# Kernel tuning notes

Measured on AMD Instinct MI355X. Metric: run time of the kernel, lower is better.

Reference implementation:

```python
import jax, jax.numpy as jnp
import numpy as np

N = 50000
ALPHA = 0.1
LAMDA = 0.5


def setup_inputs() -> dict:
    key = jax.random.key(0)
    ks = jax.random.split(key, 8)
    E, IN, H, C, L = 800000, 512, 128, 40, 8
    features = jax.random.normal(ks[0], (N, IN), dtype=jnp.float32)
    edge_index = jax.random.randint(ks[1], (2, E), 0, N, dtype=jnp.int32)
    norm_A = jax.random.uniform(ks[2], (E,), dtype=jnp.float32) * 0.1
    w_fc0 = jax.random.normal(ks[3], (IN, H), dtype=jnp.float32) / np.sqrt(IN)
    b_fc0 = jnp.zeros((H,), dtype=jnp.float32)
    conv_w = jax.random.normal(ks[4], (L, H, H), dtype=jnp.float32) / np.sqrt(H)
    w_fc1 = jax.random.normal(ks[5], (H, C), dtype=jnp.float32) / np.sqrt(H)
    b_fc1 = jnp.zeros((C,), dtype=jnp.float32)
    return {"features": features, "edge_index": edge_index, "norm_A": norm_A,
            "w_fc0": w_fc0, "b_fc0": b_fc0, "conv_w": conv_w,
            "w_fc1": w_fc1, "b_fc1": b_fc1}


def _spmm(edge_index, w, x):
    # y[dst] += w_e * x[src]  over all edges; x: [N, H]
    src, dst = edge_index[0], edge_index[1]
    msgs = x[src] * w[:, None]                      # [E, H]
    return jax.ops.segment_sum(msgs, dst, num_segments=N)


def reference(features, edge_index, norm_A, w_fc0, b_fc0, conv_w, w_fc1, b_fc1):
    # dropout p=0.0 -> identity
    x = jax.nn.relu(features @ w_fc0 + b_fc0)       # [N, H]
    h0 = x
    L = conv_w.shape[0]
    for i in range(L):
        l = i + 1
        beta = jnp.log(LAMDA / l + 1.0).astype(x.dtype)
        hi = _spmm(edge_index, norm_A, x)           # Â x
        support = (1.0 - ALPHA) * hi + ALPHA * h0   # initial residual
        # identity mapping: beta * (support W) + (1-beta) * support
        x = jax.nn.relu(beta * (support @ conv_w[i]) + (1.0 - beta) * support)
    return x @ w_fc1 + b_fc1                        # [N, C]
```

## Files before the change

### kernel.cpp

```cpp
#include <hip/hip_runtime.h>
#include <hip/hip_bf16.h>
#include <math.h>

#define N_NODES 50000
#define M_PAD   50048
#define E_EDGES 800000
#define IN_DIM  512
#define HDIM    128
#define CDIM    40
#define LAYERS  8
#define NB      196

typedef __attribute__((ext_vector_type(8))) short short8;
typedef __attribute__((ext_vector_type(4))) float floatx4;
typedef unsigned short ushort_t;

__device__ inline float bf2f(unsigned short u) {
    return __uint_as_float(((unsigned)u) << 16);
}
__device__ inline unsigned short f2bf(float v) {
    __hip_bfloat16 b = __float2bfloat16(v);
    return *reinterpret_cast<unsigned short*>(&b);
}


__global__ void hist_kernel(const int* __restrict__ dst, int* __restrict__ cnt) {
    int i = blockIdx.x * blockDim.x + threadIdx.x;
    if (i < E_EDGES) atomicAdd(&cnt[dst[i]], 1);
}

__global__ void scanA(const int* __restrict__ cnt, int* __restrict__ bsum) {
    __shared__ int sm[256];
    int t = threadIdx.x, i = blockIdx.x * 256 + t;
    sm[t] = (i < N_NODES) ? cnt[i] : 0;
    __syncthreads();
    for (int d = 128; d > 0; d >>= 1) {
        if (t < d) sm[t] += sm[t + d];
        __syncthreads();
    }
    if (t == 0) bsum[blockIdx.x] = sm[0];
}

__global__ void scanB(const int* __restrict__ bsum, int* __restrict__ boff) {
    __shared__ int sm[256];
    int t = threadIdx.x;
    sm[t] = (t < NB) ? bsum[t] : 0;
    __syncthreads();
    for (int d = 1; d < 256; d <<= 1) {
        int v = (t >= d) ? sm[t - d] : 0;
        __syncthreads();
        sm[t] += v;
        __syncthreads();
    }
    if (t < NB) boff[t] = (t > 0) ? sm[t - 1] : 0;
}

__global__ void scanC(const int* __restrict__ cnt, const int* __restrict__ boff,
                      int* __restrict__ row_start, int* __restrict__ cursor) {
    __shared__ int sm[256];
    int t = threadIdx.x, i = blockIdx.x * 256 + t;
    int v = (i < N_NODES) ? cnt[i] : 0;
    sm[t] = v;
    __syncthreads();
    for (int d = 1; d < 256; d <<= 1) {
        int x = (t >= d) ? sm[t - d] : 0;
        __syncthreads();
        sm[t] += x;
        __syncthreads();
    }
    if (i < N_NODES) {
        int incl = boff[blockIdx.x] + sm[t];
        int excl = incl - v;
        row_start[i] = excl;
        cursor[i]    = excl;
        if (i == N_NODES - 1) row_start[N_NODES] = incl;
    }
}

__global__ void scatter_kernel(const int* __restrict__ ei, const float* __restrict__ normA,
                               int* __restrict__ cursor, int2* __restrict__ perm) {
    int i = blockIdx.x * blockDim.x + threadIdx.x;
    if (i >= E_EDGES) return;
    int d = ei[E_EDGES + i];
    int idx = atomicAdd(&cursor[d], 1);
    perm[idx] = make_int2(ei[i], __float_as_int(normA[i]));
}


__global__ void prep_weights(const float* __restrict__ W0, const float* __restrict__ convW,
                             const float* __restrict__ W1,
                             ushort_t* __restrict__ Wt0, ushort_t* __restrict__ WtL,
                             ushort_t* __restrict__ Wt1) {
    int i = blockIdx.x * blockDim.x + threadIdx.x;
    if (i < 128 * 512) {
        int n = i >> 9, k = i & 511;
        Wt0[i] = f2bf(W0[k * HDIM + n]);
        return;
    }
    int j = i - 128 * 512;
    if (j < 8 * 128 * 128) {
        int l = j >> 14, rem = j & 16383, n = rem >> 7, k = rem & 127;
        WtL[j] = f2bf(convW[l * 16384 + k * HDIM + n]);
        return;
    }
    int m = j - 8 * 128 * 128;
    if (m < 48 * 128) {
        int n = m >> 7, k = m & 127;
        Wt1[m] = (n < CDIM) ? f2bf(W1[k * CDIM + n]) : (ushort_t)0;
    }
}


__global__ __launch_bounds__(256, 1)
void fc0_mfma(const float* __restrict__ F, const ushort_t* __restrict__ Wt0,
              const float* __restrict__ b0, ushort_t* __restrict__ h0b) {
    int t = threadIdx.x;
    int wave = t >> 6, lane = t & 63;
    int quad = lane >> 4, l16 = lane & 15;
    int R0 = blockIdx.x * 128 + wave * 32;

    int r0 = R0 + l16;      if (r0 > N_NODES - 1) r0 = N_NODES - 1;
    int r1 = R0 + 16 + l16; if (r1 > N_NODES - 1) r1 = N_NODES - 1;
    const float* ap0 = F + (size_t)r0 * IN_DIM + quad * 8;
    const float* ap1 = F + (size_t)r1 * IN_DIM + quad * 8;
    const ushort_t* bbase = Wt0 + (size_t)l16 * IN_DIM + quad * 8;

    floatx4 acc0[8], acc1[8];
#pragma unroll
    for (int nt = 0; nt < 8; nt++) {
        acc0[nt] = (floatx4){0.f, 0.f, 0.f, 0.f};
        acc1[nt] = (floatx4){0.f, 0.f, 0.f, 0.f};
    }

    float4 pf[8][4];
#pragma unroll
    for (int d = 0; d < 8; d++) {
        pf[d][0] = *(const float4*)(ap0 + d * 32);
        pf[d][1] = *(const float4*)(ap0 + d * 32 + 4);
        pf[d][2] = *(const float4*)(ap1 + d * 32);
        pf[d][3] = *(const float4*)(ap1 + d * 32 + 4);
    }

#pragma unroll
    for (int ks = 0; ks < 16; ks++) {
        float4 lo0 = pf[ks & 7][0], hi0 = pf[ks & 7][1];
        float4 lo1 = pf[ks & 7][2], hi1 = pf[ks & 7][3];
        short8 a0, a1;
        a0[0] = (short)f2bf(lo0.x); a0[1] = (short)f2bf(lo0.y);
        a0[2] = (short)f2bf(lo0.z); a0[3] = (short)f2bf(lo0.w);
        a0[4] = (short)f2bf(hi0.x); a0[5] = (short)f2bf(hi0.y);
        a0[6] = (short)f2bf(hi0.z); a0[7] = (short)f2bf(hi0.w);
        a1[0] = (short)f2bf(lo1.x); a1[1] = (short)f2bf(lo1.y);
        a1[2] = (short)f2bf(lo1.z); a1[3] = (short)f2bf(lo1.w);
        a1[4] = (short)f2bf(hi1.x); a1[5] = (short)f2bf(hi1.y);
        a1[6] = (short)f2bf(hi1.z); a1[7] = (short)f2bf(hi1.w);
        if (ks + 8 < 16) {
            pf[ks & 7][0] = *(const float4*)(ap0 + (ks + 8) * 32);
            pf[ks & 7][1] = *(const float4*)(ap0 + (ks + 8) * 32 + 4);
            pf[ks & 7][2] = *(const float4*)(ap1 + (ks + 8) * 32);
            pf[ks & 7][3] = *(const float4*)(ap1 + (ks + 8) * 32 + 4);
        }
#pragma unroll
        for (int nt = 0; nt < 8; nt++) {
            short8 b = *(const short8*)(bbase + (size_t)nt * 16 * IN_DIM + ks * 32);
            acc0[nt] = __builtin_amdgcn_mfma_f32_16x16x32_bf16(a0, b, acc0[nt], 0, 0, 0);
            acc1[nt] = __builtin_amdgcn_mfma_f32_16x16x32_bf16(a1, b, acc1[nt], 0, 0, 0);
        }
    }

#pragma unroll
    for (int nt = 0; nt < 8; nt++) {
        int col = nt * 16 + l16;
        float bias = b0[col];
#pragma unroll
        for (int r = 0; r < 4; r++) {
            int row = R0 + quad * 4 + r;
            float v = acc0[nt][r] + bias;
            v = v > 0.f ? v : 0.f;
            h0b[(size_t)row * HDIM + col] = f2bf(v);
        }
#pragma unroll
        for (int r = 0; r < 4; r++) {
            int row = R0 + 16 + quad * 4 + r;
            float v = acc1[nt][r] + bias;
            v = v > 0.f ? v : 0.f;
            h0b[(size_t)row * HDIM + col] = f2bf(v);
        }
    }
}


#define SROW 136

__device__ __forceinline__ void spmm_proc16(int2 pm, const ushort_t* __restrict__ xb,
                                            int sl, float* __restrict__ acc) {
#pragma unroll
    for (int j = 0; j < 16; j += 4) {
        int   s0 = __shfl(pm.x, j + 0, 16);
        int   s1 = __shfl(pm.x, j + 1, 16);
        int   s2 = __shfl(pm.x, j + 2, 16);
        int   s3 = __shfl(pm.x, j + 3, 16);
        float w0 = __int_as_float(__shfl(pm.y, j + 0, 16));
        float w1 = __int_as_float(__shfl(pm.y, j + 1, 16));
        float w2 = __int_as_float(__shfl(pm.y, j + 2, 16));
        float w3 = __int_as_float(__shfl(pm.y, j + 3, 16));
        short8 v0 = *(const short8*)(xb + (size_t)s0 * HDIM + sl * 8);
        short8 v1 = *(const short8*)(xb + (size_t)s1 * HDIM + sl * 8);
        short8 v2 = *(const short8*)(xb + (size_t)s2 * HDIM + sl * 8);
        short8 v3 = *(const short8*)(xb + (size_t)s3 * HDIM + sl * 8);
#pragma unroll
        for (int c = 0; c < 8; c++) {
            acc[c] += w0 * bf2f((ushort_t)v0[c]);
            acc[c] += w1 * bf2f((ushort_t)v1[c]);
            acc[c] += w2 * bf2f((ushort_t)v2[c]);
            acc[c] += w3 * bf2f((ushort_t)v3[c]);
        }
    }
}

__global__ __launch_bounds__(256)
void layer_fused(const int* __restrict__ row_start, const int2* __restrict__ perm,
                 const ushort_t* __restrict__ xb, const ushort_t* __restrict__ h0b,
                 const ushort_t* __restrict__ Wt, ushort_t* __restrict__ X,
                 float beta) {
    __shared__ short sS[64][SROW];
    int t = threadIdx.x;
    int wave = t >> 6, lane = t & 63;
    int grp = lane >> 4, sl = lane & 15;
    int quad = lane >> 4, l16 = lane & 15;
    int row0 = blockIdx.x * 64;
    int G = wave * 4 + grp;
    int Rg = row0 + G * 4;

    int rbv = 0;
    if (sl <= 4) {
        int idx = Rg + sl; if (idx > N_NODES) idx = N_NODES;
        rbv = row_start[idx];
    }
    int e0[4], e1[4];
#pragma unroll
    for (int r = 0; r < 4; r++) {
        e0[r] = __shfl(rbv, r, 16);
        e1[r] = __shfl(rbv, r + 1, 16);
    }

    int2 pA = make_int2(0, 0), pB = make_int2(0, 0);
    if (e0[0] + sl < e1[0])      pA = perm[e0[0] + sl];
    if (e0[0] + 16 + sl < e1[0]) pB = perm[e0[0] + 16 + sl];

#pragma unroll
    for (int r = 0; r < 4; r++) {
        int2 nA = make_int2(0, 0), nB = make_int2(0, 0);
        if (r < 3) {
            if (e0[r + 1] + sl < e1[r + 1])      nA = perm[e0[r + 1] + sl];
            if (e0[r + 1] + 16 + sl < e1[r + 1]) nB = perm[e0[r + 1] + 16 + sl];
        }

        float acc[8];
#pragma unroll
        for (int c = 0; c < 8; c++) acc[c] = 0.f;

        spmm_proc16(pA, xb, sl, acc);
        spmm_proc16(pB, xb, sl, acc);

        for (int chunk = e0[r] + 32; chunk < e1[r]; chunk += 32) {
            int2 qa = make_int2(0, 0), qb = make_int2(0, 0);
            if (chunk + sl < e1[r])      qa = perm[chunk + sl];
            if (chunk + 16 + sl < e1[r]) qb = perm[chunk + 16 + sl];
            spmm_proc16(qa, xb, sl, acc);
            spmm_proc16(qb, xb, sl, acc);
        }

        int row = Rg + r;
        short8 o;
        if (row < N_NODES) {
            short8 h = *(const short8*)(h0b + (size_t)row * HDIM + sl * 8);
#pragma unroll
            for (int c = 0; c < 8; c++)
                o[c] = (short)f2bf(0.9f * acc[c] + 0.1f * bf2f((ushort_t)h[c]));
        } else {
#pragma unroll
            for (int c = 0; c < 8; c++) o[c] = 0;
        }
        *(short8*)&sS[G * 4 + r][sl * 8] = o;

        pA = nA; pB = nB;
    }
    __syncthreads();

    short8 afrag[4];
#pragma unroll
    for (int ks = 0; ks < 4; ks++)
        afrag[ks] = *(const short8*)&sS[wave * 16 + l16][ks * 32 + quad * 8];

    floatx4 gacc[8];
#pragma unroll
    for (int nt = 0; nt < 8; nt++) {
        const ushort_t* bp = Wt + (size_t)(nt * 16 + l16) * HDIM + quad * 8;
        floatx4 c = (floatx4){0.f, 0.f, 0.f, 0.f};
#pragma unroll
        for (int ks = 0; ks < 4; ks++) {
            short8 b = *(const short8*)(bp + ks * 32);
            c = __builtin_amdgcn_mfma_f32_16x16x32_bf16(afrag[ks], b, c, 0, 0, 0);
        }
        gacc[nt] = c;
    }
    float g = 1.f - beta;
#pragma unroll
    for (int nt = 0; nt < 8; nt++) {
        int col = nt * 16 + l16;
#pragma unroll
        for (int r = 0; r < 4; r++) {
            int lrow = wave * 16 + quad * 4 + r;
            float s = bf2f((ushort_t)sS[lrow][col]);
            float v = beta * gacc[nt][r] + g * s;
            v = v > 0.f ? v : 0.f;
            X[(size_t)(row0 + lrow) * HDIM + col] = f2bf(v);
        }
    }
}


__global__ void fc1_mfma(const ushort_t* __restrict__ X, const ushort_t* __restrict__ Wt1,
                         const float* __restrict__ b1, float* __restrict__ out) {
    int wave = threadIdx.x >> 6;
    int lane = threadIdx.x & 63;
    int quad = lane >> 4, l16 = lane & 15;
    int row0 = blockIdx.x * 64 + wave * 16;

    int arow = row0 + l16; if (arow > N_NODES - 1) arow = N_NODES - 1;
    const ushort_t* ap = X + (size_t)arow * HDIM + quad * 8;
    short8 afrag[4];
#pragma unroll
    for (int ks = 0; ks < 4; ks++) afrag[ks] = *(const short8*)(ap + ks * 32);

    floatx4 acc[3];
#pragma unroll
    for (int nt = 0; nt < 3; nt++) {
        const ushort_t* bp = Wt1 + (size_t)(nt * 16 + l16) * HDIM + quad * 8;
        floatx4 c = (floatx4){0.f, 0.f, 0.f, 0.f};
#pragma unroll
        for (int ks = 0; ks < 4; ks++) {
            short8 b = *(const short8*)(bp + ks * 32);
            c = __builtin_amdgcn_mfma_f32_16x16x32_bf16(afrag[ks], b, c, 0, 0, 0);
        }
        acc[nt] = c;
    }
#pragma unroll
    for (int nt = 0; nt < 3; nt++) {
        int col = nt * 16 + l16;
        if (col < CDIM) {
            float bias = b1[col];
#pragma unroll
            for (int r = 0; r < 4; r++) {
                int row = row0 + quad * 4 + r;
                if (row < N_NODES)
                    out[(size_t)row * CDIM + col] = acc[nt][r] + bias;
            }
        }
    }
}


extern "C" void kernel_launch(void* const* d_in, const int* in_sizes, int n_in,
                              void* d_out, int out_size, void* d_ws, size_t ws_size,
                              hipStream_t stream) {
    const float* F     = (const float*)d_in[0];
    const int*   ei    = (const int*)d_in[1];
    const float* normA = (const float*)d_in[2];
    const float* W0    = (const float*)d_in[3];
    const float* b0    = (const float*)d_in[4];
    const float* convW = (const float*)d_in[5];
    const float* W1    = (const float*)d_in[6];
    const float* b1    = (const float*)d_in[7];
    float*       out   = (float*)d_out;

    ushort_t* h0b  = (ushort_t*)d_ws;
    ushort_t* xab  = h0b + (size_t)M_PAD * HDIM;
    ushort_t* xbb  = xab + (size_t)M_PAD * HDIM;
    ushort_t* Wt0  = xbb + (size_t)M_PAD * HDIM;
    ushort_t* WtL  = Wt0 + 128 * 512;
    ushort_t* Wt1  = WtL + 8 * 128 * 128;
    int*   row_start = (int*)(Wt1 + 48 * 128);
    int*   cursor    = row_start + (N_NODES + 8);
    int*   cnt       = cursor + (N_NODES + 8);
    int*   bsum      = cnt + (N_NODES + 8);
    int*   boff      = bsum + 256;
    int2*  perm      = (int2*)(boff + 256);

    hipMemsetAsync(cnt, 0, N_NODES * sizeof(int), stream);
    hist_kernel<<<(E_EDGES + 255) / 256, 256, 0, stream>>>(ei + E_EDGES, cnt);
    scanA<<<NB, 256, 0, stream>>>(cnt, bsum);
    scanB<<<1, 256, 0, stream>>>(bsum, boff);
    scanC<<<NB, 256, 0, stream>>>(cnt, boff, row_start, cursor);
    scatter_kernel<<<(E_EDGES + 255) / 256, 256, 0, stream>>>(ei, normA, cursor, perm);
    prep_weights<<<(128 * 512 + 8 * 128 * 128 + 48 * 128 + 255) / 256, 256, 0, stream>>>(
        W0, convW, W1, Wt0, WtL, Wt1);

    fc0_mfma<<<M_PAD / 128, 256, 0, stream>>>(F, Wt0, b0, h0b);

    ushort_t* ping = h0b;
    ushort_t* pong = xab;
    for (int i = 0; i < LAYERS; i++) {
        float beta = logf(0.5f / (float)(i + 1) + 1.0f);
        layer_fused<<<M_PAD / 64, 256, 0, stream>>>(
            row_start, perm, ping, h0b, WtL + (size_t)i * HDIM * HDIM, pong, beta);
        if (i == 0) { ping = xab; pong = xbb; }
        else { ushort_t* tmp = ping; ping = pong; pong = tmp; }
    }
    fc1_mfma<<<M_PAD / 64, 256, 0, stream>>>(ping, Wt1, b1, out);
}
```

Before: 691.0 us.

## Restructure fc0 GEMM to stage feature tiles in LDS via async loads

The fc0 kernel now handles 32 rows per block, with each of the four waves computing a 32-column slice, instead of 128 rows per block with each wave covering all 128 columns. Feature chunks are streamed into double-buffered, XOR-swizzled shared memory with global_load_lds. This gives many more blocks, lower per-thread register pressure, and coalesced loads, which should improve occupancy and memory-level parallelism on the 100MB feature read. In exchange it adds LDS traffic and barriers, and each block re-reads its 32-column slice of the weight matrix.

```diff
diff --git a/kernel.cpp b/kernel.cpp
--- a/kernel.cpp
+++ b/kernel.cpp
@@ -111,78 +111,91 @@
 }
 
 
-__global__ __launch_bounds__(256, 1)
+__global__ __launch_bounds__(256)
 void fc0_mfma(const float* __restrict__ F, const ushort_t* __restrict__ Wt0,
               const float* __restrict__ b0, ushort_t* __restrict__ h0b) {
+    __shared__ float sA[2][32 * 128];
     int t = threadIdx.x;
     int wave = t >> 6, lane = t & 63;
     int quad = lane >> 4, l16 = lane & 15;
-    int R0 = blockIdx.x * 128 + wave * 32;
-
-    int r0 = R0 + l16;      if (r0 > N_NODES - 1) r0 = N_NODES - 1;
-    int r1 = R0 + 16 + l16; if (r1 > N_NODES - 1) r1 = N_NODES - 1;
-    const float* ap0 = F + (size_t)r0 * IN_DIM + quad * 8;
-    const float* ap1 = F + (size_t)r1 * IN_DIM + quad * 8;
-    const ushort_t* bbase = Wt0 + (size_t)l16 * IN_DIM + quad * 8;
-
-    floatx4 acc0[8], acc1[8];
-#pragma unroll
-    for (int nt = 0; nt < 8; nt++) {
-        acc0[nt] = (floatx4){0.f, 0.f, 0.f, 0.f};
-        acc1[nt] = (floatx4){0.f, 0.f, 0.f, 0.f};
-    }
-
-    float4 pf[8][4];
-#pragma unroll
-    for (int d = 0; d < 8; d++) {
-        pf[d][0] = *(const float4*)(ap0 + d * 32);
-        pf[d][1] = *(const float4*)(ap0 + d * 32 + 4);
-        pf[d][2] = *(const float4*)(ap1 + d * 32);
-        pf[d][3] = *(const float4*)(ap1 + d * 32 + 4);
-    }
-
-#pragma unroll
-    for (int ks = 0; ks < 16; ks++) {
-        float4 lo0 = pf[ks & 7][0], hi0 = pf[ks & 7][1];
-        float4 lo1 = pf[ks & 7][2], hi1 = pf[ks & 7][3];
-        short8 a0, a1;
-        a0[0] = (short)f2bf(lo0.x); a0[1] = (short)f2bf(lo0.y);
-        a0[2] = (short)f2bf(lo0.z); a0[3] = (short)f2bf(lo0.w);
-        a0[4] = (short)f2bf(hi0.x); a0[5] = (short)f2bf(hi0.y);
-        a0[6] = (short)f2bf(hi0.z); a0[7] = (short)f2bf(hi0.w);
-        a1[0] = (short)f2bf(lo1.x); a1[1] = (short)f2bf(lo1.y);
-        a1[2] = (short)f2bf(lo1.z); a1[3] = (short)f2bf(lo1.w);
-        a1[4] = (short)f2bf(hi1.x); a1[5] = (short)f2bf(hi1.y);
-        a1[6] = (short)f2bf(hi1.z); a1[7] = (short)f2bf(hi1.w);
-        if (ks + 8 < 16) {
-            pf[ks & 7][0] = *(const float4*)(ap0 + (ks + 8) * 32);
-            pf[ks & 7][1] = *(const float4*)(ap0 + (ks + 8) * 32 + 4);
-            pf[ks & 7][2] = *(const float4*)(ap1 + (ks + 8) * 32);
-            pf[ks & 7][3] = *(const float4*)(ap1 + (ks + 8) * 32 + 4);
-        }
-#pragma unroll
-        for (int nt = 0; nt < 8; nt++) {
-            short8 b = *(const short8*)(bbase + (size_t)nt * 16 * IN_DIM + ks * 32);
-            acc0[nt] = __builtin_amdgcn_mfma_f32_16x16x32_bf16(a0, b, acc0[nt], 0, 0, 0);
-            acc1[nt] = __builtin_amdgcn_mfma_f32_16x16x32_bf16(a1, b, acc1[nt], 0, 0, 0);
-        }
-    }
-
-#pragma unroll
-    for (int nt = 0; nt < 8; nt++) {
-        int col = nt * 16 + l16;
+    int R0 = blockIdx.x * 32;
+
+    const ushort_t* bbase = Wt0 + (size_t)(wave * 32 + l16) * IN_DIM + quad * 8;
+
+    floatx4 acc[2][2];
+#pragma unroll
+    for (int rf = 0; rf < 2; rf++)
+#pragma unroll
+        for (int nt = 0; nt < 2; nt++) acc[rf][nt] = (floatx4){0.f, 0.f, 0.f, 0.f};
+
+    auto stage = [&](int cc, int buf) {
+#pragma unroll
+        for (int i = 0; i < 4; i++) {
+            int X = i * 4096 + wave * 1024 + lane * 16;
+            int row = X >> 9;
+            int colb = (X & 511) ^ ((row & 7) << 4);
+            int gr = R0 + row; if (gr > N_NODES - 1) gr = N_NODES - 1;
+            const float* src = F + (size_t)gr * IN_DIM + cc * 128 + (colb >> 2);
+            __builtin_amdgcn_global_load_lds(
+                (const __attribute__((address_space(1))) unsigned int*)src,
+                (__attribute__((address_space(3))) unsigned int*)&sA[buf][i * 1024 + wave * 256],
+                16, 0, 0);
+        }
+    };
+
+    stage(0, 0);
+
+    int mask = (l16 & 7) << 4;
+    int ib0 = ((quad << 5) ^ mask) >> 2;
+    int ib1 = (((quad << 5) | 16) ^ mask) >> 2;
+
+#pragma unroll
+    for (int cc = 0; cc < 4; cc++) {
+        __syncthreads();
+        if (cc < 3) stage(cc + 1, (cc + 1) & 1);
+        const float* bufp = &sA[cc & 1][0];
+        const float* r0p = bufp + l16 * 128;
+        const float* r1p = bufp + (l16 + 16) * 128;
+#pragma unroll
+        for (int k2 = 0; k2 < 4; k2++) {
+            int ks = cc * 4 + k2;
+            float4 f00 = *(const float4*)(r0p + k2 * 32 + ib0);
+            float4 f01 = *(const float4*)(r0p + k2 * 32 + ib1);
+            float4 f10 = *(const float4*)(r1p + k2 * 32 + ib0);
+            float4 f11 = *(const float4*)(r1p + k2 * 32 + ib1);
+            short8 a0, a1;
+            a0[0] = (short)f2bf(f00.x); a0[1] = (short)f2bf(f00.y);
+            a0[2] = (short)f2bf(f00.z); a0[3] = (short)f2bf(f00.w);
+            a0[4] = (short)f2bf(f01.x); a0[5] = (short)f2bf(f01.y);
+            a0[6] = (short)f2bf(f01.z); a0[7] = (short)f2bf(f01.w);
+            a1[0] = (short)f2bf(f10.x); a1[1] = (short)f2bf(f10.y);
+            a1[2] = (short)f2bf(f10.z); a1[3] = (short)f2bf(f10.w);
+            a1[4] = (short)f2bf(f11.x); a1[5] = (short)f2bf(f11.y);
+            a1[6] = (short)f2bf(f11.z); a1[7] = (short)f2bf(f11.w);
+#pragma unroll
+            for (int nt = 0; nt < 2; nt++) {
+                short8 b = *(const short8*)(bbase + (size_t)nt * 16 * IN_DIM + ks * 32);
+                acc[0][nt] = __builtin_amdgcn_mfma_f32_16x16x32_bf16(a0, b, acc[0][nt], 0, 0, 0);
+                acc[1][nt] = __builtin_amdgcn_mfma_f32_16x16x32_bf16(a1, b, acc[1][nt], 0, 0, 0);
+            }
+        }
+    }
+
+#pragma unroll
+    for (int nt = 0; nt < 2; nt++) {
+        int col = wave * 32 + nt * 16 + l16;
         float bias = b0[col];
 #pragma unroll
         for (int r = 0; r < 4; r++) {
             int row = R0 + quad * 4 + r;
-            float v = acc0[nt][r] + bias;
+            float v = acc[0][nt][r] + bias;
             v = v > 0.f ? v : 0.f;
             h0b[(size_t)row * HDIM + col] = f2bf(v);
         }
 #pragma unroll
         for (int r = 0; r < 4; r++) {
             int row = R0 + 16 + quad * 4 + r;
-            float v = acc1[nt][r] + bias;
+            float v = acc[1][nt][r] + bias;
             v = v > 0.f ? v : 0.f;
             h0b[(size_t)row * HDIM + col] = f2bf(v);
         }
@@ -397,7 +410,7 @@
     prep_weights<<<(128 * 512 + 8 * 128 * 128 + 48 * 128 + 255) / 256, 256, 0, stream>>>(
         W0, convW, W1, Wt0, WtL, Wt1);
 
-    fc0_mfma<<<M_PAD / 128, 256, 0, stream>>>(F, Wt0, b0, h0b);
+    fc0_mfma<<<M_PAD / 32, 256, 0, stream>>>(F, Wt0, b0, h0b);
 
     ushort_t* ping = h0b;
     ushort_t* pong = xab;
```

After: 683.6 us. No clear change (-1.1%).
